# Optimization experiments

Measured on AMD Instinct MI355X. Metric: run time of the kernel, lower is better.

## Reference

```python
import jax, jax.numpy as jnp
import numpy as np

DIM = 1024
HEADS = 16
HEAD_DIM = DIM // HEADS
SCALE = DIM ** (-0.5)  # note: module scales by full dim, not head_dim


def setup_inputs() -> dict:
    key = jax.random.key(0)
    k1, k2, k3, k4 = jax.random.split(key, 4)
    B, N = 4, 2048
    x = jax.random.normal(k1, (B, N, DIM), dtype=jnp.float32)
    # nn.Linear(dim, 3*dim, bias=False): weight [3*dim, dim]
    w_qkv = jax.random.normal(k2, (3 * DIM, DIM), dtype=jnp.float32) * (DIM ** -0.5)
    # nn.Linear(dim, dim) with bias
    w_out = jax.random.normal(k3, (DIM, DIM), dtype=jnp.float32) * (DIM ** -0.5)
    b_out = jax.random.normal(k4, (DIM,), dtype=jnp.float32) * 0.01
    return {"x": x, "w_qkv": w_qkv, "w_out": w_out, "b_out": b_out}


def reference(x, w_qkv, w_out, b_out):
    b, n, _ = x.shape
    qkv = jnp.einsum('bnd,ed->bne', x, w_qkv)  # [b, n, 3*dim]
    # rearrange 'b n (qkv h d) -> qkv b h n d'
    qkv = qkv.reshape(b, n, 3, HEADS, HEAD_DIM)
    q, k, v = (qkv[:, :, i].transpose(0, 2, 1, 3) for i in range(3))  # [b, h, n, d]
    dots = jnp.einsum('bhid,bhjd->bhij', q, k) * SCALE
    attn = jax.nn.softmax(dots, axis=-1)
    out = jnp.einsum('bhij,bhjd->bhid', attn, v)
    out = out.transpose(0, 2, 1, 3).reshape(b, n, HEADS * HEAD_DIM)  # [b, n, dim]
    return jnp.einsum('bnd,ed->bne', out, w_out) + b_out
```

## Files before the change

### kernel.cpp

```cpp
#include <hip/hip_runtime.h>

typedef __bf16 bf16_t;
typedef __bf16 bf16x2 __attribute__((ext_vector_type(2)));
typedef __bf16 bf16x4 __attribute__((ext_vector_type(4)));
typedef __bf16 bf16x8 __attribute__((ext_vector_type(8)));
typedef float floatx4 __attribute__((ext_vector_type(4)));

__device__ __forceinline__ void gll16(const void* g, void* l) {
  __builtin_amdgcn_global_load_lds(
      (const __attribute__((address_space(1))) void*)g,
      (__attribute__((address_space(3))) void*)l, 16, 0, 0);
}

__device__ __forceinline__ bf16x8 cvt8(const float4 a, const float4 b) {
  bf16x8 v;
  v[0] = (bf16_t)a.x; v[1] = (bf16_t)a.y; v[2] = (bf16_t)a.z; v[3] = (bf16_t)a.w;
  v[4] = (bf16_t)b.x; v[5] = (bf16_t)b.y; v[6] = (bf16_t)b.z; v[7] = (bf16_t)b.w;
  return v;
}

__device__ __forceinline__ int permk(int r) {
  const int u = r & 31;
  return (r & ~31) + (((u >> 2) & 3) << 3) + ((u >> 4) << 2) + (u & 3);
}

__global__ __launch_bounds__(256)
void cvt_all(const float* __restrict__ x,  bf16_t* __restrict__ xb,
             const float* __restrict__ wq, bf16_t* __restrict__ wqb,
             const float* __restrict__ wo, bf16_t* __restrict__ wob)
{
  const int bid = blockIdx.x;
  const float* s;
  bf16_t* d;
  int i;
  if (bid < 4096)      { s = x;  d = xb;  i = bid * 256 + threadIdx.x; }
  else if (bid < 5632) { s = wq; d = wqb; i = (bid - 4096) * 256 + threadIdx.x; }
  else                 { s = wo; d = wob; i = (bid - 5632) * 256 + threadIdx.x; }
  const float4 a = ((const float4*)s)[2 * i];
  const float4 b = ((const float4*)s)[2 * i + 1];
  *(bf16x8*)(d + (size_t)i * 8) = cvt8(a, b);
}

template<bool C32>
__global__ __launch_bounds__(256, 3)
void gemm_bt(const bf16_t* __restrict__ Ab, const bf16_t* __restrict__ Wb,
             const float* __restrict__ bias, void* __restrict__ Cv,
             int M, int Nf, int K, int lda, int qcols, float qscale)
{
  __shared__ __align__(16) bf16_t lA[3][128 * 32];
  __shared__ __align__(16) bf16_t lB[3][128 * 32];

  const int tid  = threadIdx.x;
  const int wave = tid >> 6;
  const int lane = tid & 63;
  const int q    = lane >> 4;
  const int ln   = lane & 15;
  const int wm   = wave >> 1, wn = wave & 1;

  const int x     = blockIdx.x & 7;
  const int local = blockIdx.x >> 3;
  const int mt = x * 8 + (local & 7);
  const int nt = local >> 3;
  const int m0 = mt << 7, n0 = nt << 7;

  const int kiters = K >> 5;

  auto stage = [&](int buf, int k0s) {
#pragma unroll
    for (int tt = 0; tt < 2; ++tt) {
      const int rbase = tt * 64 + wave * 16;
      const int r  = rbase + (lane >> 2);
      const int gc = (lane & 3) ^ ((r >> 1) & 3);
      gll16(Ab + (size_t)(m0 + r) * lda + k0s + gc * 8, lA[buf] + rbase * 32);
      gll16(Wb + (size_t)(n0 + r) * K   + k0s + gc * 8, lB[buf] + rbase * 32);
    }
  };

  floatx4 acc[4][4] = {};

  stage(0, 0);
  stage(1, 32);

  for (int t = 0; t < kiters; ++t) {
    const int buf = t % 3;

    if (t + 1 < kiters) {
      asm volatile("s_waitcnt vmcnt(4)" ::: "memory");
    } else {
      asm volatile("s_waitcnt vmcnt(0)" ::: "memory");
    }
    __builtin_amdgcn_sched_barrier(0);
    __builtin_amdgcn_s_barrier();
    __builtin_amdgcn_sched_barrier(0);

    bf16x8 af[4], bfr[4];
#pragma unroll
    for (int i = 0; i < 4; ++i) {
      const int r = wm * 64 + i * 16 + ln;
      af[i] = *(const bf16x8*)(lA[buf] + r * 32 + (q ^ ((r >> 1) & 3)) * 8);
    }
#pragma unroll
    for (int j = 0; j < 4; ++j) {
      const int r = wn * 64 + j * 16 + ln;
      bfr[j] = *(const bf16x8*)(lB[buf] + r * 32 + (q ^ ((r >> 1) & 3)) * 8);
    }
    __builtin_amdgcn_s_setprio(1);
#pragma unroll
    for (int i = 0; i < 4; ++i)
#pragma unroll
      for (int j = 0; j < 4; ++j)
        acc[i][j] = __builtin_amdgcn_mfma_f32_16x16x32_bf16(af[i], bfr[j], acc[i][j], 0, 0, 0);
    __builtin_amdgcn_s_setprio(0);

    if (t + 2 < kiters) stage((t + 2) % 3, (t + 2) << 5);
  }

#pragma unroll
  for (int j = 0; j < 4; ++j) {
    const int col = n0 + wn * 64 + j * 16 + ln;
    const float bv = bias ? bias[col] : 0.0f;
    const float sc = (col < qcols) ? qscale : 1.0f;
#pragma unroll
    for (int i = 0; i < 4; ++i) {
      const int row = m0 + wm * 64 + i * 16 + q * 4;
#pragma unroll
      for (int r = 0; r < 4; ++r) {
        const float val = acc[i][j][r] * sc + bv;
        if constexpr (C32)
          ((float*)Cv)[(size_t)(row + r) * Nf + col] = val;
        else
          ((bf16_t*)Cv)[(size_t)(row + r) * Nf + col] = (bf16_t)val;
      }
    }
  }
}

__global__ __launch_bounds__(256, 2)
void attn_kernel(bf16_t* __restrict__ qkv)
{
  __shared__ __align__(16) bf16_t lK[2][128 * 64];
  __shared__ __align__(16) bf16_t lVT[64 * 128];

  const int tid  = threadIdx.x;
  const int wave = tid >> 6;
  const int lane = tid & 63;
  const int q  = lane >> 4;
  const int ln = lane & 15;
  const int wm = wave >> 1, wn = wave & 1;

  const int hw = blockIdx.x;
  const int w  = (hw & 7) * 128 + (hw >> 3);
  const int qt = w & 15;
  const int h  = (w >> 4) & 15;
  const int b  = w >> 8;

  bf16_t* Qbase = qkv + (size_t)(b * 2048 + qt * 128) * 3072 + h * 64;
  const bf16_t* Kbase = qkv + (size_t)(b * 2048) * 3072 + 1024 + h * 64;
  const bf16_t* Vbase = qkv + (size_t)(b * 2048) * 3072 + 2048 + h * 64;

#pragma unroll
  for (int t = 0; t < 4; ++t) {
    const int rbase = t * 32 + wave * 8;
    const int r  = rbase + (lane >> 3);
    const int gc = (lane & 7) ^ (r & 7);
    gll16(Qbase + (size_t)r * 3072 + gc * 8, lVT + rbase * 64);
    gll16(Kbase + (size_t)permk(r) * 3072 + gc * 8, lK[0] + rbase * 64);
  }
  __syncthreads();

  bf16x8 qf[4][2];
#pragma unroll
  for (int i = 0; i < 4; ++i) {
    const int r = wm * 64 + i * 16 + ln;
#pragma unroll
    for (int kt = 0; kt < 2; ++kt) {
      const int c = (kt * 4 + q) ^ (r & 7);
      qf[i][kt] = *(const bf16x8*)(lVT + r * 64 + c * 8);
    }
  }

  bf16x8 vcur[2][2], vnxt[2][2];
#pragma unroll
  for (int it = 0; it < 2; ++it) {
    const bf16_t* src = Vbase + (size_t)(2 * lane) * 3072 + (wave + it * 4) * 8;
    vcur[it][0] = *(const bf16x8*)src;
    vcur[it][1] = *(const bf16x8*)(src + 3072);
  }

  floatx4 accO[4][4] = {};
  floatx4 accS[4] = {};

  bf16x8 ones;
#pragma unroll
  for (int j = 0; j < 8; ++j) ones[j] = (bf16_t)1.0f;

  for (int jt = 0; jt < 16; ++jt) {
    const bf16_t* lKc = lK[jt & 1];
    bf16_t*       lKn = lK[(jt & 1) ^ 1];

    __syncthreads();

#pragma unroll
    for (int it = 0; it < 2; ++it) {
      const int c = wave + it * 4;
#pragma unroll
      for (int j = 0; j < 8; ++j) {
        const int d  = c * 8 + j;
        const int ch = (lane >> 2) ^ (d & 7);
        bf16x2 pr;
        pr[0] = vcur[it][0][j];
        pr[1] = vcur[it][1][j];
        *(bf16x2*)(lVT + d * 128 + ch * 8 + ((2 * lane) & 7)) = pr;
      }
    }

    if (jt < 15) {
      const int j0n = (jt + 1) * 128;
#pragma unroll
      for (int t = 0; t < 4; ++t) {
        const int rbase = t * 32 + wave * 8;
        const int r  = rbase + (lane >> 3);
        const int gc = (lane & 7) ^ (r & 7);
        gll16(Kbase + (size_t)(j0n + permk(r)) * 3072 + gc * 8, lKn + rbase * 64);
      }
#pragma unroll
      for (int it = 0; it < 2; ++it) {
        const bf16_t* src = Vbase + (size_t)(j0n + 2 * lane) * 3072 + (wave + it * 4) * 8;
        vnxt[it][0] = *(const bf16x8*)src;
        vnxt[it][1] = *(const bf16x8*)(src + 3072);
      }
    }

    bf16x8 ap[2][4];
    __builtin_amdgcn_s_setprio(1);
#pragma unroll
    for (int c = 0; c < 2; ++c) {
#pragma unroll
      for (int e = 0; e < 2; ++e) {
        const int rb = wn * 64 + (c * 2 + e) * 16 + ln;
        const bf16x8 kf0 = *(const bf16x8*)(lKc + rb * 64 + ((q)     ^ (rb & 7)) * 8);
        const bf16x8 kf1 = *(const bf16x8*)(lKc + rb * 64 + ((4 + q) ^ (rb & 7)) * 8);
#pragma unroll
        for (int n = 0; n < 4; ++n) {
          floatx4 st = {0.0f, 0.0f, 0.0f, 0.0f};
          st = __builtin_amdgcn_mfma_f32_16x16x32_bf16(kf0, qf[n][0], st, 0, 0, 0);
          st = __builtin_amdgcn_mfma_f32_16x16x32_bf16(kf1, qf[n][1], st, 0, 0, 0);
#pragma unroll
          for (int r4 = 0; r4 < 4; ++r4)
            ap[c][n][e * 4 + r4] = (bf16_t)__builtin_amdgcn_exp2f(st[r4]);
        }
      }
    }
    __builtin_amdgcn_s_setprio(0);

    __syncthreads();

    __builtin_amdgcn_s_setprio(1);
#pragma unroll
    for (int c = 0; c < 2; ++c) {
      bf16x8 bv[4];
#pragma unroll
      for (int nd = 0; nd < 4; ++nd) {
        const int d  = nd * 16 + ln;
        const int cc = (wn * 8 + c * 4 + q) ^ (d & 7);
        bv[nd] = *(const bf16x8*)(lVT + d * 128 + cc * 8);
      }
#pragma unroll
      for (int n = 0; n < 4; ++n) {
#pragma unroll
        for (int nd = 0; nd < 4; ++nd)
          accO[n][nd] = __builtin_amdgcn_mfma_f32_16x16x32_bf16(ap[c][n], bv[nd], accO[n][nd], 0, 0, 0);
        accS[n] = __builtin_amdgcn_mfma_f32_16x16x32_bf16(ap[c][n], ones, accS[n], 0, 0, 0);
      }
    }
    __builtin_amdgcn_s_setprio(0);

    if (jt < 15) {
#pragma unroll
      for (int it = 0; it < 2; ++it) {
        vcur[it][0] = vnxt[it][0];
        vcur[it][1] = vnxt[it][1];
      }
    }
  }

  float* red  = (float*)lK;
  float* redS = (float*)lVT;

  if (wn == 1) {
#pragma unroll
    for (int n = 0; n < 4; ++n)
#pragma unroll
      for (int nd = 0; nd < 4; ++nd)
#pragma unroll
        for (int r4 = 0; r4 < 4; ++r4)
          red[wm * 4096 + (n * 16 + q * 4 + r4) * 64 + nd * 16 + ln] = accO[n][nd][r4];
  }
  __syncthreads();
  if (wn == 1 && ln == 0) {
#pragma unroll
    for (int n = 0; n < 4; ++n)
#pragma unroll
      for (int r4 = 0; r4 < 4; ++r4)
        redS[wm * 64 + n * 16 + q * 4 + r4] = accS[n][r4];
  }
  __syncthreads();
  if (wn == 0) {
#pragma unroll
    for (int n = 0; n < 4; ++n) {
#pragma unroll
      for (int r4 = 0; r4 < 4; ++r4) {
        const int m = n * 16 + q * 4 + r4;
        const float s = accS[n][r4] + redS[wm * 64 + m];
        const float rcp = 1.0f / fmaxf(s, 1e-20f);
#pragma unroll
        for (int nd = 0; nd < 4; ++nd) {
          const float o = accO[n][nd][r4] + red[wm * 4096 + m * 64 + nd * 16 + ln];
          Qbase[(size_t)(wm * 64 + m) * 3072 + nd * 16 + ln] = (bf16_t)(o * rcp);
        }
      }
    }
  }
}

extern "C" void kernel_launch(void* const* d_in, const int* in_sizes, int n_in,
                              void* d_out, int out_size, void* d_ws, size_t ws_size,
                              hipStream_t stream)
{
  const float* x     = (const float*)d_in[0];
  const float* w_qkv = (const float*)d_in[1];
  const float* w_out = (const float*)d_in[2];
  const float* b_out = (const float*)d_in[3];
  float* out = (float*)d_out;

  bf16_t* qkv    = (bf16_t*)d_ws;
  bf16_t* xb     = qkv    + (size_t)8192 * 3072;
  bf16_t* wqkvb  = xb     + (size_t)8192 * 1024;
  bf16_t* woutb  = wqkvb  + (size_t)3072 * 1024;

  const float qs = 0.04508422f;

  cvt_all<<<dim3(6144), dim3(256), 0, stream>>>(x, xb, w_qkv, wqkvb, w_out, woutb);

  gemm_bt<false><<<dim3(64 * 24), dim3(256), 0, stream>>>(
      xb, wqkvb, nullptr, qkv, 8192, 3072, 1024, 1024, 1024, qs);
  attn_kernel<<<dim3(1024), dim3(256), 0, stream>>>(qkv);
  gemm_bt<true><<<dim3(64 * 8), dim3(256), 0, stream>>>(
      qkv, woutb, b_out, out, 8192, 1024, 1024, 3072, 0, 1.0f);
}
```

Baseline: 259.0 us.

## Enlarge GEMM tiles to 256x256x64 with 512-thread blocks and double buffering

The projection GEMM is retiled from 128x128 tiles with a 32-wide K step, three LDS buffers and 4 waves to 256x256 tiles with a 64-wide K step, two LDS buffers and 8 waves. Each wave now computes a 128x64 sub-tile. The LDS swizzle is changed to fit the 64-wide rows, and an extra barrier is added before refilling the buffer just consumed. The aim is more reuse per byte loaded and fewer K iterations. In exchange, each block uses about 128KB of LDS, so only one block fits per CU. The grids also shrink to 384 and 128 blocks, which can leave CUs idle or unevenly loaded, especially in the output projection.

```diff
diff --git a/kernel.cpp b/kernel.cpp
--- a/kernel.cpp
+++ b/kernel.cpp
@@ -42,50 +42,52 @@
 }
 
 template<bool C32>
-__global__ __launch_bounds__(256, 3)
+__global__ __launch_bounds__(512)
 void gemm_bt(const bf16_t* __restrict__ Ab, const bf16_t* __restrict__ Wb,
              const float* __restrict__ bias, void* __restrict__ Cv,
              int M, int Nf, int K, int lda, int qcols, float qscale)
 {
-  __shared__ __align__(16) bf16_t lA[3][128 * 32];
-  __shared__ __align__(16) bf16_t lB[3][128 * 32];
+  __shared__ __align__(16) bf16_t lA[2][256 * 64];
+  __shared__ __align__(16) bf16_t lB[2][256 * 64];
 
   const int tid  = threadIdx.x;
   const int wave = tid >> 6;
   const int lane = tid & 63;
   const int q    = lane >> 4;
   const int ln   = lane & 15;
-  const int wm   = wave >> 1, wn = wave & 1;
-
-  const int x     = blockIdx.x & 7;
-  const int local = blockIdx.x >> 3;
-  const int mt = x * 8 + (local & 7);
-  const int nt = local >> 3;
-  const int m0 = mt << 7, n0 = nt << 7;
-
-  const int kiters = K >> 5;
+  const int wm2  = wave >> 2;
+  const int wn2  = wave & 3;
+
+  const int x      = blockIdx.x & 7;
+  const int local  = blockIdx.x >> 3;
+  const int mchunk = (M >> 8) >> 3;
+  const int mt = x * mchunk + (local % mchunk);
+  const int nt = local / mchunk;
+  const int m0 = mt << 8, n0 = nt << 8;
+
+  const int kiters = K >> 6;
 
   auto stage = [&](int buf, int k0s) {
 #pragma unroll
-    for (int tt = 0; tt < 2; ++tt) {
-      const int rbase = tt * 64 + wave * 16;
-      const int r  = rbase + (lane >> 2);
-      const int gc = (lane & 3) ^ ((r >> 1) & 3);
-      gll16(Ab + (size_t)(m0 + r) * lda + k0s + gc * 8, lA[buf] + rbase * 32);
-      gll16(Wb + (size_t)(n0 + r) * K   + k0s + gc * 8, lB[buf] + rbase * 32);
+    for (int rr = 0; rr < 4; ++rr) {
+      const int rbase = rr * 64 + wave * 8;
+      const int r  = rbase + (lane >> 3);
+      const int gc = (lane & 7) ^ (r & 7);
+      gll16(Ab + (size_t)(m0 + r) * lda + k0s + gc * 8, lA[buf] + rbase * 64);
+      gll16(Wb + (size_t)(n0 + r) * K   + k0s + gc * 8, lB[buf] + rbase * 64);
     }
   };
 
-  floatx4 acc[4][4] = {};
+  floatx4 acc[8][4] = {};
 
   stage(0, 0);
-  stage(1, 32);
+  if (kiters > 1) stage(1, 64);
 
   for (int t = 0; t < kiters; ++t) {
-    const int buf = t % 3;
+    const int buf = t & 1;
 
     if (t + 1 < kiters) {
-      asm volatile("s_waitcnt vmcnt(4)" ::: "memory");
+      asm volatile("s_waitcnt vmcnt(8)" ::: "memory");
     } else {
       asm volatile("s_waitcnt vmcnt(0)" ::: "memory");
     }
@@ -93,36 +95,43 @@
     __builtin_amdgcn_s_barrier();
     __builtin_amdgcn_sched_barrier(0);
 
-    bf16x8 af[4], bfr[4];
-#pragma unroll
-    for (int i = 0; i < 4; ++i) {
-      const int r = wm * 64 + i * 16 + ln;
-      af[i] = *(const bf16x8*)(lA[buf] + r * 32 + (q ^ ((r >> 1) & 3)) * 8);
-    }
+    bf16x8 bfr[4][2];
 #pragma unroll
     for (int j = 0; j < 4; ++j) {
-      const int r = wn * 64 + j * 16 + ln;
-      bfr[j] = *(const bf16x8*)(lB[buf] + r * 32 + (q ^ ((r >> 1) & 3)) * 8);
+      const int r = wn2 * 64 + j * 16 + ln;
+#pragma unroll
+      for (int kt = 0; kt < 2; ++kt) {
+        const int c = (kt * 4 + q) ^ (r & 7);
+        bfr[j][kt] = *(const bf16x8*)(lB[buf] + r * 64 + c * 8);
+      }
     }
     __builtin_amdgcn_s_setprio(1);
 #pragma unroll
-    for (int i = 0; i < 4; ++i)
-#pragma unroll
-      for (int j = 0; j < 4; ++j)
-        acc[i][j] = __builtin_amdgcn_mfma_f32_16x16x32_bf16(af[i], bfr[j], acc[i][j], 0, 0, 0);
+    for (int i = 0; i < 8; ++i) {
+      const int r = wm2 * 128 + i * 16 + ln;
+      const bf16x8 af0 = *(const bf16x8*)(lA[buf] + r * 64 + ((q)     ^ (r & 7)) * 8);
+      const bf16x8 af1 = *(const bf16x8*)(lA[buf] + r * 64 + ((4 + q) ^ (r & 7)) * 8);
+#pragma unroll
+      for (int j = 0; j < 4; ++j) {
+        acc[i][j] = __builtin_amdgcn_mfma_f32_16x16x32_bf16(af0, bfr[j][0], acc[i][j], 0, 0, 0);
+        acc[i][j] = __builtin_amdgcn_mfma_f32_16x16x32_bf16(af1, bfr[j][1], acc[i][j], 0, 0, 0);
+      }
+    }
     __builtin_amdgcn_s_setprio(0);
 
-    if (t + 2 < kiters) stage((t + 2) % 3, (t + 2) << 5);
+    __builtin_amdgcn_s_barrier();
+    __builtin_amdgcn_sched_barrier(0);
+    if (t + 2 < kiters) stage(buf, (t + 2) << 6);
   }
 
 #pragma unroll
   for (int j = 0; j < 4; ++j) {
-    const int col = n0 + wn * 64 + j * 16 + ln;
+    const int col = n0 + wn2 * 64 + j * 16 + ln;
     const float bv = bias ? bias[col] : 0.0f;
     const float sc = (col < qcols) ? qscale : 1.0f;
 #pragma unroll
-    for (int i = 0; i < 4; ++i) {
-      const int row = m0 + wm * 64 + i * 16 + q * 4;
+    for (int i = 0; i < 8; ++i) {
+      const int row = m0 + wm2 * 128 + i * 16 + q * 4;
 #pragma unroll
       for (int r = 0; r < 4; ++r) {
         const float val = acc[i][j][r] * sc + bv;
@@ -342,9 +351,9 @@
 
   cvt_all<<<dim3(6144), dim3(256), 0, stream>>>(x, xb, w_qkv, wqkvb, w_out, woutb);
 
-  gemm_bt<false><<<dim3(64 * 24), dim3(256), 0, stream>>>(
+  gemm_bt<false><<<dim3(384), dim3(512), 0, stream>>>(
       xb, wqkvb, nullptr, qkv, 8192, 3072, 1024, 1024, 1024, qs);
   attn_kernel<<<dim3(1024), dim3(256), 0, stream>>>(qkv);
-  gemm_bt<true><<<dim3(64 * 8), dim3(256), 0, stream>>>(
+  gemm_bt<true><<<dim3(128), dim3(512), 0, stream>>>(
       qkv, woutb, b_out, out, 8192, 1024, 1024, 3072, 0, 1.0f);
 }
```

New measurement: 282.3 us. 9.0% more time.
